# Kernel optimization log

Hardware: AMD Instinct MI355X
Metric: run time of the kernel (lower is better)

Reference implementation:

```python
import jax, jax.numpy as jnp
import numpy as np


def setup_inputs() -> dict:
    key = jax.random.key(0)
    ks = jax.random.split(key, 9)
    B, C, H, W, D = 2, 64, 64, 64, 16
    Cq = C // 8
    return {
        "x2d": jax.random.normal(ks[0], (B, C, H, W, D), jnp.float32),
        "x3d": jax.random.normal(ks[1], (B, C, H, W, D), jnp.float32),
        "Wq": jax.random.normal(ks[2], (Cq, C), jnp.float32) * 0.05,
        "bq": jax.random.normal(ks[3], (Cq,), jnp.float32) * 0.05,
        "Wk": jax.random.normal(ks[4], (Cq, C), jnp.float32) * 0.05,
        "bk": jax.random.normal(ks[5], (Cq,), jnp.float32) * 0.05,
        "Wv": jax.random.normal(ks[6], (C, C), jnp.float32) * 0.05,
        "bv": jax.random.normal(ks[7], (C,), jnp.float32) * 0.05,
        "gamma": jax.random.normal(ks[8], (1,), jnp.float32),
    }


def reference(x2d, x3d, Wq, bq, Wk, bk, Wv, bv, gamma):
    # x2d/x3d: (B, C, H, W, D) -> permute to (B, C, D, H, W)
    xp = jnp.transpose(x2d, (0, 1, 4, 2, 3))
    B, C, D, H, W = xp.shape
    N = H * W

    # 1x1x1 Conv3d == channel contraction
    q = jnp.einsum('oc,bcdhw->bodhw', Wq, xp) + bq[None, :, None, None, None]
    k = jnp.einsum('oc,bcdhw->bodhw', Wk, xp) + bk[None, :, None, None, None]
    v = jnp.einsum('oc,bcdhw->bodhw', Wv, xp) + bv[None, :, None, None, None]

    # fold depth into feature dim; attention over N = H*W positions
    pq = q.reshape(B, -1, N)                  # (B, Cq*D, N)
    pk = k.reshape(B, -1, N)                  # (B, Cq*D, N)
    energy = jnp.einsum('bcn,bcm->bnm', pq, pk)   # (B, N, N)
    attn = jax.nn.softmax(energy, axis=-1)

    pv = v.reshape(B, -1, N)                  # (B, C*D, N)
    # out[b,c,n] = sum_m pv[b,c,m] * attn[b,n,m]
    out = jnp.einsum('bcm,bnm->bcn', pv, attn)
    out = out.reshape(B, C, D, H, W)
    out = jnp.transpose(out, (0, 1, 3, 4, 2))  # back to (B, C, H, W, D)
    return gamma * out + x3d
```

## Files before the change

kernel.cpp:

```cpp
#include <hip/hip_runtime.h>
#include <hip/hip_bf16.h>

typedef __attribute__((ext_vector_type(8))) short short8;
typedef __attribute__((ext_vector_type(8))) __bf16 bf16x8;
typedef __attribute__((ext_vector_type(4))) float f32x4;

#define N_   4096
#define CQD  128
#define CVD  1024
#define PLD  136

static __device__ __forceinline__ unsigned short f2bf(float f) {
    union { float f; unsigned int u; } cv; cv.f = f;
    unsigned int u = cv.u;
    u += 0x7fffu + ((u >> 16) & 1u);
    return (unsigned short)(u >> 16);
}

static __device__ __forceinline__ f32x4 mfma16(bf16x8 a, bf16x8 b, f32x4 c) {
    return __builtin_amdgcn_mfma_f32_16x16x32_bf16(a, b, c, 0, 0, 0);
}

__global__ __launch_bounds__(256) void proj_kernel(
    const float* __restrict__ x2d,
    const float* __restrict__ Wq, const float* __restrict__ bq,
    const float* __restrict__ Wk, const float* __restrict__ bk,
    const float* __restrict__ Wv, const float* __restrict__ bv,
    unsigned short* __restrict__ Qb, unsigned short* __restrict__ Kb,
    unsigned short* __restrict__ PV)
{
    const int t  = threadIdx.x;
    const int blk = blockIdx.x;
    const int b  = blk >> 8;
    const int n0 = (blk & 255) << 4;
    const int n  = t & 15;
    const int dd = t >> 4;

    const float* xb = x2d + ((size_t)b * 64 * N_ + (size_t)(n0 + n)) * 16 + dd;
    float xr[64];
#pragma unroll
    for (int c = 0; c < 64; ++c) xr[c] = xb[(size_t)c * (N_ * 16)];

    unsigned short* pvb = PV + (size_t)b * CVD * N_;
    for (int j = 0; j < 64; ++j) {
        float acc = bv[j];
#pragma unroll
        for (int c = 0; c < 64; ++c) acc += Wv[j * 64 + c] * xr[c];
        pvb[(size_t)(j * 16 + dd) * N_ + n0 + n] = f2bf(acc);
    }
    unsigned short* qb = Qb + (size_t)b * N_ * CQD;
    unsigned short* kb = Kb + (size_t)b * N_ * CQD;
    for (int j = 0; j < 8; ++j) {
        float aq = bq[j], ak = bk[j];
#pragma unroll
        for (int c = 0; c < 64; ++c) {
            float xv = xr[c];
            aq += Wq[j * 64 + c] * xv;
            ak += Wk[j * 64 + c] * xv;
        }
        qb[(size_t)(n0 + n) * CQD + j * 16 + dd] = f2bf(aq);
        kb[(size_t)(n0 + n) * CQD + j * 16 + dd] = f2bf(ak);
    }
}

__global__ __launch_bounds__(512, 2) void attn_kernel(
    const unsigned short* __restrict__ Qb, const unsigned short* __restrict__ Kb,
    const unsigned short* __restrict__ PV,
    const float* __restrict__ x3d, const float* __restrict__ gamma_p,
    float* __restrict__ outp)
{
    __shared__ unsigned short p_lds[2][64][PLD];
    __shared__ float red[64];

    const int t  = threadIdx.x;
    const int w  = t >> 6;
    const int l  = t & 63;
    const int lo = l & 15;
    const int hi = l >> 4;

    const int id    = blockIdx.x;
    const int combo = (id >> 1) & 3;
    const int chalf = combo & 1;
    const int b     = combo >> 1;
    const int xl    = ((id >> 3) << 1) | (id & 1);
    const int n0    = xl << 6;
    const int cw    = (chalf << 9) + (w << 6);
    const int g     = w >> 2;
    const int msel  = w & 3;

    const unsigned short* qp  = Qb + (size_t)b * N_ * CQD;
    const unsigned short* kp  = Kb + (size_t)b * N_ * CQD;
    const unsigned short* pvp = PV + (size_t)b * CVD * N_;

    bf16x8 qf[2][4];
#pragma unroll
    for (int ns = 0; ns < 2; ++ns)
#pragma unroll
        for (int kk = 0; kk < 4; ++kk)
            qf[ns][kk] = *reinterpret_cast<const bf16x8*>(
                qp + (size_t)(n0 + g * 32 + ns * 16 + lo) * CQD + kk * 32 + hi * 8);

    f32x4 acc[4][4];
#pragma unroll
    for (int i = 0; i < 4; ++i)
#pragma unroll
        for (int j = 0; j < 4; ++j) acc[i][j] = (f32x4){0.f, 0.f, 0.f, 0.f};
    float rs[8];
#pragma unroll
    for (int i = 0; i < 8; ++i) rs[i] = 0.f;

    if (t < 64) red[t] = 0.f;

    for (int it = 0; it < 32; ++it) {
        const int m0  = it << 7;
        const int buf = it & 1;
        const int mc  = m0 + (msel << 5);

        bf16x8 kf[2][4];
#pragma unroll
        for (int ms = 0; ms < 2; ++ms)
#pragma unroll
            for (int kk = 0; kk < 4; ++kk)
                kf[ms][kk] = *reinterpret_cast<const bf16x8*>(
                    kp + (size_t)(mc + ms * 16 + lo) * CQD + kk * 32 + hi * 8);
        f32x4 e[2][2];
#pragma unroll
        for (int ns = 0; ns < 2; ++ns)
#pragma unroll
            for (int ms = 0; ms < 2; ++ms) {
                f32x4 ee = (f32x4){0.f, 0.f, 0.f, 0.f};
#pragma unroll
                for (int kk = 0; kk < 4; ++kk) ee = mfma16(qf[ns][kk], kf[ms][kk], ee);
                e[ns][ms] = ee;
            }
#pragma unroll
        for (int ns = 0; ns < 2; ++ns)
#pragma unroll
            for (int ms = 0; ms < 2; ++ms)
#pragma unroll
                for (int r = 0; r < 4; ++r) {
                    float p = __expf(e[ns][ms][r]);
                    rs[ns * 4 + r] += p;
                    p_lds[buf][g * 32 + ns * 16 + hi * 4 + r][(msel << 5) + ms * 16 + lo] = f2bf(p);
                }
        __syncthreads();

#pragma unroll
        for (int kk = 0; kk < 4; ++kk) {
            bf16x8 af[4];
#pragma unroll
            for (int ns = 0; ns < 4; ++ns)
                af[ns] = *reinterpret_cast<const bf16x8*>(&p_lds[buf][ns * 16 + lo][kk * 32 + hi * 8]);
            bf16x8 bvv[4];
#pragma unroll
            for (int cs = 0; cs < 4; ++cs)
                bvv[cs] = *reinterpret_cast<const bf16x8*>(
                    pvp + (size_t)(cw + cs * 16 + lo) * N_ + m0 + kk * 32 + hi * 8);
#pragma unroll
            for (int ns = 0; ns < 4; ++ns)
#pragma unroll
                for (int cs = 0; cs < 4; ++cs)
                    acc[ns][cs] = mfma16(af[ns], bvv[cs], acc[ns][cs]);
        }
    }

#pragma unroll
    for (int i = 0; i < 8; ++i) {
        float v = rs[i];
        v += __shfl_xor(v, 1);
        v += __shfl_xor(v, 2);
        v += __shfl_xor(v, 4);
        v += __shfl_xor(v, 8);
        rs[i] = v;
    }
    if (lo == 0) {
#pragma unroll
        for (int ns = 0; ns < 2; ++ns)
#pragma unroll
            for (int r = 0; r < 4; ++r)
                atomicAdd(&red[g * 32 + ns * 16 + hi * 4 + r], rs[ns * 4 + r]);
    }
    __syncthreads();

    const float gmv = gamma_p[0];
    const float* x3p = x3d + (size_t)b * 64 * N_ * 16;
    float* op        = outp + (size_t)b * 64 * N_ * 16;
#pragma unroll
    for (int ns = 0; ns < 4; ++ns) {
        float rinv[4];
#pragma unroll
        for (int r = 0; r < 4; ++r) rinv[r] = 1.0f / red[ns * 16 + hi * 4 + r];
#pragma unroll
        for (int cs = 0; cs < 4; ++cs) {
            const int cp = cw + cs * 16 + lo;
            const size_t base = (size_t)(cp >> 4) * (N_ * 16) + (size_t)(cp & 15);
#pragma unroll
            for (int r = 0; r < 4; ++r) {
                const size_t idx = base + (size_t)(n0 + ns * 16 + hi * 4 + r) * 16;
                op[idx] = gmv * acc[ns][cs][r] * rinv[r] + x3p[idx];
            }
        }
    }
}

extern "C" void kernel_launch(void* const* d_in, const int* in_sizes, int n_in,
                              void* d_out, int out_size, void* d_ws, size_t ws_size,
                              hipStream_t stream)
{
    const float* x2d = (const float*)d_in[0];
    const float* x3d = (const float*)d_in[1];
    const float* Wq  = (const float*)d_in[2];
    const float* bq  = (const float*)d_in[3];
    const float* Wk  = (const float*)d_in[4];
    const float* bk  = (const float*)d_in[5];
    const float* Wv  = (const float*)d_in[6];
    const float* bv  = (const float*)d_in[7];
    const float* gm  = (const float*)d_in[8];

    char* ws = (char*)d_ws;
    unsigned short* Qb = (unsigned short*)ws;
    unsigned short* Kb = (unsigned short*)(ws + (2u << 20));
    unsigned short* PV = (unsigned short*)(ws + (4u << 20));

    proj_kernel<<<512, 256, 0, stream>>>(x2d, Wq, bq, Wk, bk, Wv, bv, Qb, Kb, PV);
    attn_kernel<<<256, 512, 0, stream>>>(Qb, Kb, PV, x3d, gm, (float*)d_out);
}
```

Before: 382.8 us.

## Restructure projection with LDS staging and prefetch PV loads, swizzle P buffer

The projection kernel now stages x tiles in LDS with coalesced loads. Warp groups split the Q/K and V outputs, and V results are transposed through LDS so PV rows are written as 16-byte vectors. The attention kernel issues all PV global loads before the QK^T MFMAs so their latency overlaps the softmax work. It also replaces the padded P buffer with an XOR-swizzled layout to avoid bank conflicts. In exchange, register pressure rises from holding 16 PV fragments, and the projection uses uneven work splits with divergent barriers across branches.

Measured after the change: 334.8 us. -12.5%, faster.

```diff
diff --git a/kernel.cpp b/kernel.cpp
--- a/kernel.cpp
+++ b/kernel.cpp
@@ -7,8 +7,6 @@
 
 #define N_   4096
 #define CQD  128
-#define CVD  1024
-#define PLD  136
 
 static __device__ __forceinline__ unsigned short f2bf(float f) {
     union { float f; unsigned int u; } cv; cv.f = f;
@@ -21,7 +19,7 @@
     return __builtin_amdgcn_mfma_f32_16x16x32_bf16(a, b, c, 0, 0, 0);
 }
 
-__global__ __launch_bounds__(256) void proj_kernel(
+__global__ __launch_bounds__(512) void proj_kernel(
     const float* __restrict__ x2d,
     const float* __restrict__ Wq, const float* __restrict__ bq,
     const float* __restrict__ Wk, const float* __restrict__ bk,
@@ -29,37 +27,81 @@
     unsigned short* __restrict__ Qb, unsigned short* __restrict__ Kb,
     unsigned short* __restrict__ PV)
 {
-    const int t  = threadIdx.x;
-    const int blk = blockIdx.x;
-    const int b  = blk >> 8;
-    const int n0 = (blk & 255) << 4;
-    const int n  = t & 15;
-    const int dd = t >> 4;
-
-    const float* xb = x2d + ((size_t)b * 64 * N_ + (size_t)(n0 + n)) * 16 + dd;
-    float xr[64];
-#pragma unroll
-    for (int c = 0; c < 64; ++c) xr[c] = xb[(size_t)c * (N_ * 16)];
-
-    unsigned short* pvb = PV + (size_t)b * CVD * N_;
-    for (int j = 0; j < 64; ++j) {
-        float acc = bv[j];
-#pragma unroll
-        for (int c = 0; c < 64; ++c) acc += Wv[j * 64 + c] * xr[c];
-        pvb[(size_t)(j * 16 + dd) * N_ + n0 + n] = f2bf(acc);
-    }
-    unsigned short* qb = Qb + (size_t)b * N_ * CQD;
-    unsigned short* kb = Kb + (size_t)b * N_ * CQD;
-    for (int j = 0; j < 8; ++j) {
-        float aq = bq[j], ak = bk[j];
-#pragma unroll
+    __shared__ char smem[32768];
+    float*          xlds = (float*)smem;
+    unsigned short* vout = (unsigned short*)smem;
+
+    const int t    = threadIdx.x;
+    const int blk  = blockIdx.x;
+    const int b    = blk >> 9;
+    const int tile = blk & 511;
+    const int col0 = tile << 7;
+    const int jg   = __builtin_amdgcn_readfirstlane(t >> 7);
+    const int tl   = t & 127;
+    const int dd   = tl & 15;
+    const int nl   = tl >> 4;
+    const int col  = col0 + tl;
+    const int n    = col >> 4;
+
+    const float* xb = x2d + (size_t)b * 64 * 65536 + col0;
+#pragma unroll
+    for (int i = 0; i < 16; ++i) {
+        const int idx = (i << 9) + t;
+        xlds[idx] = xb[(size_t)(idx >> 7) * 65536 + (idx & 127)];
+    }
+    __syncthreads();
+
+    if (jg == 0) {
+        float aq[8], ak[8];
+#pragma unroll
+        for (int j = 0; j < 8; ++j) { aq[j] = bq[j]; ak[j] = bk[j]; }
+#pragma unroll 16
         for (int c = 0; c < 64; ++c) {
-            float xv = xr[c];
-            aq += Wq[j * 64 + c] * xv;
-            ak += Wk[j * 64 + c] * xv;
-        }
-        qb[(size_t)(n0 + n) * CQD + j * 16 + dd] = f2bf(aq);
-        kb[(size_t)(n0 + n) * CQD + j * 16 + dd] = f2bf(ak);
+            const float xv = xlds[c * 128 + tl];
+#pragma unroll
+            for (int j = 0; j < 8; ++j) {
+                aq[j] += Wq[j * 64 + c] * xv;
+                ak[j] += Wk[j * 64 + c] * xv;
+            }
+        }
+        unsigned short* qb = Qb + (size_t)b * N_ * CQD + (size_t)n * CQD + dd;
+        unsigned short* kb = Kb + (size_t)b * N_ * CQD + (size_t)n * CQD + dd;
+#pragma unroll
+        for (int j = 0; j < 8; ++j) {
+            qb[j * 16] = f2bf(aq[j]);
+            kb[j * 16] = f2bf(ak[j]);
+        }
+        __syncthreads();
+        __syncthreads();
+    } else {
+        const int v0 = (jg - 1) * 22;
+        int wr[22];
+#pragma unroll
+        for (int j = 0; j < 22; ++j) wr[j] = (v0 + j < 64) ? (v0 + j) : 63;
+        float av[22];
+#pragma unroll
+        for (int j = 0; j < 22; ++j) av[j] = bv[wr[j]];
+#pragma unroll 16
+        for (int c = 0; c < 64; ++c) {
+            const float xv = xlds[c * 128 + tl];
+#pragma unroll
+            for (int j = 0; j < 22; ++j) av[j] += Wv[wr[j] * 64 + c] * xv;
+        }
+        __syncthreads();
+#pragma unroll
+        for (int j = 0; j < 22; ++j) {
+            if (v0 + j < 64)
+                vout[(size_t)(((v0 + j) << 4) + dd) * 8 + nl] = f2bf(av[j]);
+        }
+        __syncthreads();
+    }
+
+    unsigned short* pvb = PV + (size_t)b * 1024 * N_ + (tile << 3);
+#pragma unroll
+    for (int i = 0; i < 2; ++i) {
+        const int r = t + (i << 9);
+        const short8 v = *reinterpret_cast<const short8*>(vout + r * 8);
+        *reinterpret_cast<short8*>(pvb + (size_t)r * N_) = v;
     }
 }
 
@@ -69,7 +111,7 @@
     const float* __restrict__ x3d, const float* __restrict__ gamma_p,
     float* __restrict__ outp)
 {
-    __shared__ unsigned short p_lds[2][64][PLD];
+    __shared__ char pbuf[2][64 * 256];
     __shared__ float red[64];
 
     const int t  = threadIdx.x;
@@ -90,7 +132,7 @@
 
     const unsigned short* qp  = Qb + (size_t)b * N_ * CQD;
     const unsigned short* kp  = Kb + (size_t)b * N_ * CQD;
-    const unsigned short* pvp = PV + (size_t)b * CVD * N_;
+    const unsigned short* pvp = PV + (size_t)b * 1024 * N_;
 
     bf16x8 qf[2][4];
 #pragma unroll
@@ -123,44 +165,53 @@
             for (int kk = 0; kk < 4; ++kk)
                 kf[ms][kk] = *reinterpret_cast<const bf16x8*>(
                     kp + (size_t)(mc + ms * 16 + lo) * CQD + kk * 32 + hi * 8);
-        f32x4 e[2][2];
-#pragma unroll
-        for (int ns = 0; ns < 2; ++ns)
-#pragma unroll
-            for (int ms = 0; ms < 2; ++ms) {
-                f32x4 ee = (f32x4){0.f, 0.f, 0.f, 0.f};
-#pragma unroll
-                for (int kk = 0; kk < 4; ++kk) ee = mfma16(qf[ns][kk], kf[ms][kk], ee);
-                e[ns][ms] = ee;
-            }
-#pragma unroll
-        for (int ns = 0; ns < 2; ++ns)
-#pragma unroll
-            for (int ms = 0; ms < 2; ++ms)
-#pragma unroll
-                for (int r = 0; r < 4; ++r) {
-                    float p = __expf(e[ns][ms][r]);
-                    rs[ns * 4 + r] += p;
-                    p_lds[buf][g * 32 + ns * 16 + hi * 4 + r][(msel << 5) + ms * 16 + lo] = f2bf(p);
-                }
+        bf16x8 bvv[4][4];
+#pragma unroll
+        for (int kk = 0; kk < 4; ++kk)
+#pragma unroll
+            for (int cs = 0; cs < 4; ++cs)
+                bvv[kk][cs] = *reinterpret_cast<const bf16x8*>(
+                    pvp + (size_t)(cw + cs * 16 + lo) * N_ + m0 + kk * 32 + hi * 8);
+
+        char* pb = pbuf[buf];
+#pragma unroll
+        for (int ms = 0; ms < 2; ++ms) {
+            f32x4 e0 = (f32x4){0.f, 0.f, 0.f, 0.f};
+            f32x4 e1 = (f32x4){0.f, 0.f, 0.f, 0.f};
+#pragma unroll
+            for (int kk = 0; kk < 4; ++kk) {
+                e0 = mfma16(qf[0][kk], kf[ms][kk], e0);
+                e1 = mfma16(qf[1][kk], kf[ms][kk], e1);
+            }
+            const int colb = ((msel << 5) + ms * 16 + lo) * 2;
+#pragma unroll
+            for (int r = 0; r < 4; ++r) {
+                const float p0 = __expf(e0[r]);
+                const float p1 = __expf(e1[r]);
+                rs[r]     += p0;
+                rs[4 + r] += p1;
+                const int row0 = g * 32 + hi * 4 + r;
+                const int row1 = row0 + 16;
+                *(unsigned short*)(pb + row0 * 256 + (colb ^ ((row0 & 15) << 4))) = f2bf(p0);
+                *(unsigned short*)(pb + row1 * 256 + (colb ^ ((row1 & 15) << 4))) = f2bf(p1);
+            }
+        }
         __syncthreads();
 
 #pragma unroll
         for (int kk = 0; kk < 4; ++kk) {
             bf16x8 af[4];
 #pragma unroll
+            for (int ns = 0; ns < 4; ++ns) {
+                const int row = ns * 16 + lo;
+                af[ns] = *reinterpret_cast<const bf16x8*>(
+                    pb + row * 256 + ((kk * 64 + hi * 16) ^ ((row & 15) << 4)));
+            }
+#pragma unroll
             for (int ns = 0; ns < 4; ++ns)
-                af[ns] = *reinterpret_cast<const bf16x8*>(&p_lds[buf][ns * 16 + lo][kk * 32 + hi * 8]);
-            bf16x8 bvv[4];
-#pragma unroll
-            for (int cs = 0; cs < 4; ++cs)
-                bvv[cs] = *reinterpret_cast<const bf16x8*>(
-                    pvp + (size_t)(cw + cs * 16 + lo) * N_ + m0 + kk * 32 + hi * 8);
-#pragma unroll
-            for (int ns = 0; ns < 4; ++ns)
 #pragma unroll
                 for (int cs = 0; cs < 4; ++cs)
-                    acc[ns][cs] = mfma16(af[ns], bvv[cs], acc[ns][cs]);
+                    acc[ns][cs] = mfma16(af[ns], bvv[kk][cs], acc[ns][cs]);
         }
     }
 
@@ -222,6 +273,6 @@
     unsigned short* Kb = (unsigned short*)(ws + (2u << 20));
     unsigned short* PV = (unsigned short*)(ws + (4u << 20));
 
-    proj_kernel<<<512, 256, 0, stream>>>(x2d, Wq, bq, Wk, bk, Wv, bv, Qb, Kb, PV);
+    proj_kernel<<<1024, 512, 0, stream>>>(x2d, Wq, bq, Wk, bk, Wv, bv, Qb, Kb, PV);
     attn_kernel<<<256, 512, 0, stream>>>(Qb, Kb, PV, x3d, gm, (float*)d_out);
 }
```
